# Performance work log

Hardware: AMD Instinct MI355X
Metric: run time of the kernel (lower is better)

Reference implementation:

```python
import jax, jax.numpy as jnp
import numpy as np

B, T, Nt = 64, 256, 77      # batch, motion length, text tokens
H, L = 8, 64                # num_heads, latent_dim per head
D = H * L                   # 512 model dim
Pt = 256                    # text_latent_dim
Ht = 1                      # num_text_heads
E, K = 8, 2                 # num_experts, topk
TEMB = 2048                 # time_embed_dim
MAXS, MAXTS = 512, 77       # max_seq_len, max_text_seq_len
NEG = -1e6


def _ln(x, g, b, eps=1e-5):
    m = jnp.mean(x, -1, keepdims=True)
    v = jnp.mean((x - m) ** 2, -1, keepdims=True)
    return (x - m) * jax.lax.rsqrt(v + eps) * g + b


def _gelu(x):
    return jax.nn.gelu(x, approximate=False)


def _moe_tokens(x, gate_w, fc1w, fc1b, fc2w, fc2b):
    # top-k softmax gate (fp32) + expert FFNs; dense compute, sparse combine.
    logits = x.astype(jnp.float32) @ gate_w.astype(jnp.float32)          # [Ntok,E]
    gates = jax.nn.softmax(logits, axis=-1)
    topv, topi = jax.lax.top_k(gates, K)
    topv = topv / jnp.sum(topv, -1, keepdims=True)
    dense = jnp.sum(jax.nn.one_hot(topi, E, dtype=topv.dtype) * topv[..., None], axis=1)
    dense = dense.astype(x.dtype)                                        # [Ntok,E]
    y = jnp.zeros((x.shape[0], fc2w.shape[-1]), x.dtype)
    for e in range(E):  # small fixed expert loop
        h = _gelu(x @ fc1w[e] + fc1b[e])
        y = y + dense[:, e:e + 1] * (h @ fc2w[e] + fc2b[e])
    return y


def _moe_block(x, pos, gate_w, fc1w, fc1b, fc2w, fc2b, projw, projb):
    # x: [B,Tn,Hn,Din]; add learned positional embedding, MoE over tokens, GELU, proj.
    b, t, h, d = x.shape
    x = x + pos[:, :t]
    y = _moe_tokens(x.reshape(-1, d), gate_w, fc1w, fc1b, fc2w, fc2b)
    y = _gelu(y) @ projw + projb
    return y.reshape(b, t, h, -1)


def _fwd(x, xf, emb, src_mask, norm_g, norm_b, tnorm_g, tnorm_b, m_pos, m_gate, m_fc1w, m_fc1b, m_fc2w, m_fc2b, m_projw, m_projb, t_pos, t_gate, t_fc1w, t_fc1b, t_fc2w, t_fc2b, t_projw, t_projb, body_w, sb_embw, sb_embb, sb_ng, sb_nb, sb_outw, sb_outb, cond_type):
    Bx, Tx, Dx = x.shape
    x4 = x.reshape(Bx, Tx, H, L)
    tf = xf.reshape(Bx, Nt, Ht, Pt)
    text_feat = _moe_block(_ln(tf, tnorm_g, tnorm_b), t_pos, t_gate, t_fc1w, t_fc1b, t_fc2w, t_fc2b, t_projw, t_projb)      # [B,Nt,Ht,2L]
    motion_feat = _moe_block(_ln(x4, norm_g, norm_b), m_pos, m_gate, m_fc1w, m_fc1b, m_fc2w, m_fc2b, m_projw, m_projb)      # [B,T,H,4L]
    # static body-part mixing
    bw = jax.nn.softmax(body_w, axis=1)
    body_feat = jnp.einsum('hl,bnld->bnhd', bw, motion_feat[..., :L]).reshape(Bx, Tx, Dx)
    tc = (cond_type % 10 > 0).astype(x.dtype).reshape(Bx, 1, 1, 1)
    sm = src_mask.reshape(Bx, Tx, 1, 1)
    key_text = jnp.broadcast_to(text_feat[..., :L] + (1.0 - tc) * NEG, (Bx, Nt, H, L))
    key_motion = motion_feat[..., L:2 * L] + (1.0 - sm) * NEG
    key = jax.nn.softmax(jnp.concatenate([key_text, key_motion], axis=1), axis=1)  # softmax over N
    val_text = jnp.broadcast_to(text_feat[..., L:] * tc, (Bx, Nt, H, L))
    val_motion = motion_feat[..., 2 * L:3 * L] * sm
    value = jnp.concatenate([val_text, val_motion], axis=1)                        # [B,N,H,L]
    query = jax.nn.softmax(motion_feat[..., 3 * L:], axis=-1)                      # [B,T,H,L]
    attn = jnp.einsum('bnhd,bnhl->bhdl', key, value)                               # [B,H,L,L]
    y_t = jnp.einsum('bnhd,bhdl->bnhl', query, attn).reshape(Bx, Tx, Dx)
    # StylizationBlock (eval: dropout is identity)
    h = _ln(body_feat + y_t, sb_ng, sb_nb)
    eo = jax.nn.silu(emb) @ sb_embw + sb_embb                                      # [B,2D]
    h = h * (1.0 + eo[:, None, :Dx]) + eo[:, None, Dx:]
    h = jax.nn.silu(h) @ sb_outw + sb_outb
    return x + h


def setup_inputs() -> dict:
    ks = iter(jax.random.split(jax.random.key(0), 48))
    nrm = lambda shape, s: jax.random.normal(next(ks), shape, jnp.float32) * s
    return {
        "x": nrm((B, T, D), 1.0),
        "xf": nrm((B, Nt, Pt), 1.0),
        "emb": nrm((B, TEMB), 1.0),
        "src_mask": jnp.ones((B, T, 1), jnp.float32),
        "norm_g": jnp.ones((L,), jnp.float32), "norm_b": jnp.zeros((L,), jnp.float32),
        "tnorm_g": jnp.ones((Pt,), jnp.float32), "tnorm_b": jnp.zeros((Pt,), jnp.float32),
        "m_pos": nrm((1, MAXS, H, L), 0.02),
        "m_gate": nrm((L, E), 0.02),
        "m_fc1w": nrm((E, L, 4 * L), 0.02), "m_fc1b": jnp.zeros((E, 4 * L), jnp.float32),
        "m_fc2w": nrm((E, 4 * L, L), 0.02), "m_fc2b": jnp.zeros((E, L), jnp.float32),
        "m_projw": nrm((L, 4 * L), 0.02), "m_projb": jnp.zeros((4 * L,), jnp.float32),
        "t_pos": nrm((1, MAXTS, Ht, Pt), 0.02),
        "t_gate": nrm((Pt, E), 0.02),
        "t_fc1w": nrm((E, Pt, 4 * Pt), 0.02), "t_fc1b": jnp.zeros((E, 4 * Pt), jnp.float32),
        "t_fc2w": nrm((E, 4 * Pt, Pt), 0.02), "t_fc2b": jnp.zeros((E, Pt), jnp.float32),
        "t_projw": nrm((Pt, 2 * L), 0.02), "t_projb": jnp.zeros((2 * L,), jnp.float32),
        "body_w": nrm((H, H), 1.0),
        "sb_embw": nrm((TEMB, 2 * D), 0.02), "sb_embb": jnp.zeros((2 * D,), jnp.float32),
        "sb_ng": jnp.ones((D,), jnp.float32), "sb_nb": jnp.zeros((D,), jnp.float32),
        "sb_outw": nrm((D, D), 0.02), "sb_outb": jnp.zeros((D,), jnp.float32),
        "cond_type": jax.random.randint(next(ks), (B, 1, 1), 0, 100, jnp.int32),
        "motion_length": T,
        "num_intervals": 1,
    }


def reference(x, xf, emb, src_mask, norm_g, norm_b, tnorm_g, tnorm_b, m_pos, m_gate, m_fc1w, m_fc1b, m_fc2w, m_fc2b, m_projw, m_projb, t_pos, t_gate, t_fc1w, t_fc1b, t_fc2w, t_fc2b, t_projw, t_projb, body_w, sb_embw, sb_embb, sb_ng, sb_nb, sb_outw, sb_outb, cond_type, motion_length, num_intervals):
    # motion_length / num_intervals are unused by the forward math (as in the source).
    return _fwd(x, xf, emb, src_mask, norm_g, norm_b, tnorm_g, tnorm_b, m_pos, m_gate, m_fc1w, m_fc1b, m_fc2w, m_fc2b, m_projw, m_projb, t_pos, t_gate, t_fc1w, t_fc1b, t_fc2w, t_fc2b, t_projw, t_projb, body_w, sb_embw, sb_embb, sb_ng, sb_nb, sb_outw, sb_outb, cond_type)
```

## Files before the change

kernel.cpp:

```cpp
#include <hip/hip_runtime.h>
#include <hip/hip_bf16.h>


typedef __hip_bfloat16 bf16;
typedef unsigned short u16;
typedef unsigned int   u32;
typedef __attribute__((ext_vector_type(8))) short short8;
typedef __attribute__((ext_vector_type(4))) short s16x4;
typedef __attribute__((ext_vector_type(4))) float f32x4;

#define MFMA16(a,b,c) __builtin_amdgcn_mfma_f32_16x16x32_bf16(a,b,c,0,0,0)

__device__ __forceinline__ float b2f(bf16 v){ return __bfloat162float(v); }
__device__ __forceinline__ u16 f2bu(float f){
  union { __hip_bfloat16 hh; u16 us; } cv; cv.hh = __float2bfloat16(f); return cv.us;
}
__device__ __forceinline__ float bu2f(u16 v){ return __uint_as_float(((u32)v)<<16); }

__device__ __forceinline__ float geluf(float x){
  float t = x*x;
  float w = x * fmaf(-0.10294453f, t, -2.3022077f);
  float z = exp2f(w);
  return x * __builtin_amdgcn_rcpf(1.f + z);
}
__device__ __forceinline__ float siluf(float x){
  float z = exp2f(-1.442695f * x);
  return x * __builtin_amdgcn_rcpf(1.f + z);
}

__device__ __forceinline__ float wsum(float v){
#pragma unroll
  for (int o=32;o>0;o>>=1) v += __shfl_xor(v,o,64);
  return v;
}
__device__ __forceinline__ float wmax(float v){
#pragma unroll
  for (int o=32;o>0;o>>=1) v = fmaxf(v, __shfl_xor(v,o,64));
  return v;
}
__device__ __forceinline__ void top2(const float* lg, int& i1, int& i2, float& wA){
  i1 = 0; float v1 = lg[0];
#pragma unroll
  for (int e=1;e<8;e++) if (lg[e] > v1){ v1 = lg[e]; i1 = e; }
  i2 = 0; float v2 = -1e30f;
#pragma unroll
  for (int e=0;e<8;e++) if (e != i1 && lg[e] > v2){ v2 = lg[e]; i2 = e; }
  wA = 1.f/(1.f + expf(v2 - v1));
}

__device__ __forceinline__ float sum2_wave(float x, int b0){
  float s = x, ss = x*x;
  float v = (b0 ? ss : s) + __shfl_xor(b0 ? s : ss, 1, 64);
  v += __shfl_xor(v, 2, 64);
  v += __shfl_xor(v, 4, 64);
  v += __shfl_xor(v, 8, 64);
  v += __shfl_xor(v, 16, 64);
  v += __shfl_xor(v, 32, 64);
  return v;
}

__device__ __forceinline__ float rsum8(const float p[8], int lane){
  int b0 = lane & 1, b1 = lane & 2, b2 = lane & 4;
  float w[4], u[2], v;
#pragma unroll
  for (int j=0;j<4;j++){
    float keep = b0 ? p[2*j+1] : p[2*j];
    float send = b0 ? p[2*j]   : p[2*j+1];
    w[j] = keep + __shfl_xor(send, 1, 64);
  }
#pragma unroll
  for (int i=0;i<2;i++){
    float keep = b1 ? w[2*i+1] : w[2*i];
    float send = b1 ? w[2*i]   : w[2*i+1];
    u[i] = keep + __shfl_xor(send, 2, 64);
  }
  {
    float keep = b2 ? u[1] : u[0];
    float send = b2 ? u[0] : u[1];
    v = keep + __shfl_xor(send, 4, 64);
  }
  v += __shfl_xor(v, 8, 64);
  v += __shfl_xor(v, 16, 64);
  v += __shfl_xor(v, 32, 64);
  return v;
}

__device__ __forceinline__ short8 ld8(const u16* p){
  s16x4 lo = *(const s16x4*)p;
  s16x4 hi = *(const s16x4*)(p + 4);
  short8 r;
  r[0]=lo[0]; r[1]=lo[1]; r[2]=lo[2]; r[3]=lo[3];
  r[4]=hi[0]; r[5]=hi[1]; r[6]=hi[2]; r[7]=hi[3];
  return r;
}

__global__ __launch_bounds__(64) void k_zero(int* cnts){ cnts[threadIdx.x] = 0; }

__global__ __launch_bounds__(64) void k_bw(const float* __restrict__ body_w, float* __restrict__ bwv){
  int t = threadIdx.x;
  if (t < 8){
    float v[8]; float mx = -1e30f;
#pragma unroll
    for (int j=0;j<8;j++){ v[j] = body_w[t*8+j]; mx = fmaxf(mx, v[j]); }
    float s = 0.f;
#pragma unroll
    for (int j=0;j<8;j++){ v[j] = expf(v[j]-mx); s += v[j]; }
#pragma unroll
    for (int j=0;j<8;j++) bwv[t*8+j] = v[j]/s;
  }
}

__global__ __launch_bounds__(256) void k_repack(const float* __restrict__ s, u16* __restrict__ d,
                                                int KC, int N, int total){
  int NT = N >> 4;
  for (int t = blockIdx.x*256 + threadIdx.x; t < total; t += gridDim.x*256){
    int j = t & 7, n = (t>>3) & 15, q = (t>>7) & 3;
    int r2 = t >> 9;
    int kc = r2 % KC; int r3 = r2 / KC;
    int nt = r3 % NT; int e = r3 / NT;
    int k = kc*32 + q*8 + j;
    d[t] = f2bu(s[((size_t)(e*(KC*32) + k))*N + nt*16 + n]);
  }
}

__global__ __launch_bounds__(256) void k_count(const int2* __restrict__ eidx, int n, int* __restrict__ cnt){
  __shared__ int h[8];
  int tid = threadIdx.x;
  if (tid < 8) h[tid] = 0;
  __syncthreads();
  for (int i = blockIdx.x*256 + tid; i < n; i += gridDim.x*256){
    int2 e = eidx[i];
    atomicAdd(&h[e.x], 1); atomicAdd(&h[e.y], 1);
  }
  __syncthreads();
  if (tid < 8) atomicAdd(&cnt[tid], h[tid]);
}

__global__ __launch_bounds__(64) void k_scan(int* cnts){
  if (threadIdx.x == 0){
    int s = 0;
    for (int e=0;e<8;e++){ cnts[16+e] = s; cnts[32+e] = s; s += cnts[e]; }
    s = 0;
    for (int e=0;e<8;e++){ cnts[24+e] = s; cnts[40+e] = s; s += cnts[8+e]; }
  }
}

__global__ __launch_bounds__(256) void k_fill(const int2* __restrict__ eidx, int n,
                                              int* __restrict__ off2, int* __restrict__ alist){
  __shared__ int lc[8], gb[8], lc2[8];
  int tid = threadIdx.x;
  if (tid < 8){ lc[tid] = 0; lc2[tid] = 0; }
  __syncthreads();
  for (int i = blockIdx.x*256 + tid; i < n; i += gridDim.x*256){
    int2 e = eidx[i];
    atomicAdd(&lc[e.x], 1); atomicAdd(&lc[e.y], 1);
  }
  __syncthreads();
  if (tid < 8) gb[tid] = atomicAdd(&off2[tid], lc[tid]);
  __syncthreads();
  for (int i = blockIdx.x*256 + tid; i < n; i += gridDim.x*256){
    int2 e = eidx[i];
    int s0 = atomicAdd(&lc2[e.x], 1); alist[gb[e.x] + s0] = i*2;
    int s1 = atomicAdd(&lc2[e.y], 1); alist[gb[e.y] + s1] = i*2 + 1;
  }
}

__global__ __launch_bounds__(256) void k_text_pre(
    const float* __restrict__ xf, const float* __restrict__ tg, const float* __restrict__ tb,
    const float* __restrict__ tpos, const float* __restrict__ gw,
    u16* __restrict__ xtb, int2* __restrict__ eidxT, float2* __restrict__ ewT){
  int tok = blockIdx.x, tid = threadIdx.x;
  int n = tok % 77;
  __shared__ float redw[32], lgs[8];
  int w = tid >> 6, ln = tid & 63;
  int b0 = tid & 1;
  float xv = xf[tok*256 + tid];
  float v = sum2_wave(xv, b0);
  if (ln < 2) redw[w*2 + ln] = v;
  __syncthreads();
  float mean = (redw[0]+redw[2]+redw[4]+redw[6]) * (1.f/256.f);
  float var  = (redw[1]+redw[3]+redw[5]+redw[7]) * (1.f/256.f) - mean*mean;
  float r = rsqrtf(var + 1e-5f);
  float xn = (xv - mean)*r*tg[tid] + tb[tid] + tpos[n*256 + tid];
  xtb[tok*256 + tid] = f2bu(xn);
  float p[8];
#pragma unroll
  for (int e=0;e<8;e++) p[e] = xn * gw[tid*8 + e];
  float vv = rsum8(p, ln);
  __syncthreads();
  if (ln < 8) redw[w*8 + ln] = vv;
  __syncthreads();
  if (tid < 8) lgs[tid] = redw[tid] + redw[8+tid] + redw[16+tid] + redw[24+tid];
  __syncthreads();
  if (tid == 0){
    int i1, i2; float wA; top2(lgs, i1, i2, wA);
    eidxT[tok] = make_int2(i1, i2);
    ewT[tok] = make_float2(wA, 1.f - wA);
  }
}

__global__ __launch_bounds__(256) void k_motion_pre(
    const float* __restrict__ x, const float* __restrict__ ng, const float* __restrict__ nb,
    const float* __restrict__ mpos, const float* __restrict__ gw,
    u16* __restrict__ xmb, int2* __restrict__ eidxM, float2* __restrict__ ewM){
  int tok = blockIdx.x*4 + (threadIdx.x >> 6);
  int d = threadIdx.x & 63;
  int b0 = d & 1;
  float xv = x[(size_t)tok*64 + d];
  float v = sum2_wave(xv, b0);
  float o = __shfl_xor(v, 1, 64);
  float sf  = b0 ? o : v;
  float ssf = b0 ? v : o;
  float mean = sf * (1.f/64.f);
  float var  = ssf * (1.f/64.f) - mean*mean;
  float r = rsqrtf(var + 1e-5f);
  int h = tok & 7; int t = (tok >> 3) & 255;
  float xn = (xv - mean)*r*ng[d] + nb[d] + mpos[(t*8+h)*64 + d];
  xmb[(size_t)tok*64 + d] = f2bu(xn);
  float p[8];
#pragma unroll
  for (int e=0;e<8;e++) p[e] = xn * gw[d*8 + e];
  float vv = rsum8(p, d);
  float lg[8];
#pragma unroll
  for (int e=0;e<8;e++) lg[e] = __shfl(vv, e, 64);
  if (d == 0){
    int i1, i2; float wA; top2(lg, i1, i2, wA);
    eidxM[tok] = make_int2(i1, i2);
    ewM[tok] = make_float2(wA, 1.f - wA);
  }
}

__global__ __launch_bounds__(256) void k_motion_moe(
    const u16* __restrict__ xmb, const int* __restrict__ alistM, const int* __restrict__ cnts,
    const u16* __restrict__ w1pk, const float* __restrict__ fc1b,
    const u16* __restrict__ w2pk, const float* __restrict__ fc2b,
    u16* __restrict__ ycM){
  int e = blockIdx.y, tile = blockIdx.x, tid = threadIdx.x;
  int cnt = cnts[8+e]; int base = tile*32;
  if (base >= cnt) return;
  int nn = min(32, cnt - base); int off = cnts[24+e];
  __shared__ int toks[32];
  __shared__ u16 xs[32*72];
  __shared__ u16 hT[32*264];
  if (tid < 32) toks[tid] = alistM[off + base + min(tid, nn-1)];
  __syncthreads();
  { int row = tid >> 3, c0 = (tid & 7)*8;
    short8 v = *(const short8*)(xmb + (size_t)(toks[row]>>1)*64 + c0);
    *(short8*)&xs[row*72 + c0] = v; }
  __syncthreads();
  int lane = tid & 63, w = tid >> 6;
  int n = lane & 15, q = lane >> 4;
  int mt = w & 1;
  short8 a0 = *(const short8*)&xs[(mt*16 + n)*72 + q*8];
  short8 a1 = *(const short8*)&xs[(mt*16 + n)*72 + 32 + q*8];
  const short8* b1 = (const short8*)(w1pk + (size_t)e*16384);
#pragma unroll
  for (int i=0;i<8;i++){
    int nt = (w>>1)*8 + i;
    f32x4 acc = {0.f,0.f,0.f,0.f};
    acc = MFMA16(a0, b1[(nt*2+0)*64 + lane], acc);
    acc = MFMA16(a1, b1[(nt*2+1)*64 + lane], acc);
    float bias = fc1b[e*256 + nt*16 + n];
#pragma unroll
    for (int r=0;r<4;r++)
      hT[(mt*16 + q*4 + r)*264 + nt*16 + n] = f2bu(geluf(acc[r] + bias));
  }
  __syncthreads();
  short8 a2[8];
#pragma unroll
  for (int kc=0;kc<8;kc++) a2[kc] = *(const short8*)&hT[(mt*16 + n)*264 + kc*32 + q*8];
  const short8* b2 = (const short8*)(w2pk + (size_t)e*16384);
#pragma unroll
  for (int i=0;i<2;i++){
    int nt = (w>>1)*2 + i;
    f32x4 acc = {0.f,0.f,0.f,0.f};
#pragma unroll
    for (int kc=0;kc<8;kc++) acc = MFMA16(a2[kc], b2[(nt*8+kc)*64 + lane], acc);
    float bias = fc2b[e*64 + nt*16 + n];
#pragma unroll
    for (int r=0;r<4;r++){
      int row = mt*16 + q*4 + r;
      if (row < nn) ycM[(size_t)toks[row]*64 + nt*16 + n] = f2bu(acc[r] + bias);
    }
  }
}

__global__ __launch_bounds__(256) void k_text_moe(
    const u16* __restrict__ xtb, const int* __restrict__ alistT, const int* __restrict__ cnts,
    const u16* __restrict__ w1pk, const float* __restrict__ fc1b,
    const u16* __restrict__ w2pk, const float* __restrict__ fc2b,
    float* __restrict__ ycT){
  int e = blockIdx.y, tile = blockIdx.x, tid = threadIdx.x;
  int cnt = cnts[e]; int base = tile*16;
  if (base >= cnt) return;
  int nn = min(16, cnt - base); int off = cnts[16+e];
  __shared__ int toks[16];
  __shared__ u16 xs[16*280];
  __shared__ u16 hT[16*1048];
  if (tid < 16) toks[tid] = alistT[off + base + min(tid, nn-1)];
  __syncthreads();
  { int row = tid >> 4, c0 = (tid & 15)*16;
    const short8* sp = (const short8*)(xtb + (size_t)(toks[row]>>1)*256 + c0);
    short8 v0 = sp[0], v1 = sp[1];
    *(short8*)&xs[row*280 + c0] = v0;
    *(short8*)&xs[row*280 + c0 + 8] = v1; }
  __syncthreads();
  int lane = tid & 63, w = tid >> 6;
  int n = lane & 15, q = lane >> 4;
  short8 a_[8];
#pragma unroll
  for (int kc=0;kc<8;kc++) a_[kc] = *(const short8*)&xs[n*280 + kc*32 + q*8];
  const short8* b1 = (const short8*)(w1pk + (size_t)e*262144);
#pragma unroll 1
  for (int i=0;i<16;i++){
    int nt = w*16 + i;
    f32x4 acc = {0.f,0.f,0.f,0.f};
#pragma unroll
    for (int kc=0;kc<8;kc++) acc = MFMA16(a_[kc], b1[(nt*8+kc)*64 + lane], acc);
    float bias = fc1b[e*1024 + nt*16 + n];
#pragma unroll
    for (int r=0;r<4;r++)
      hT[(q*4 + r)*1048 + nt*16 + n] = f2bu(geluf(acc[r] + bias));
  }
  __syncthreads();
  const short8* b2 = (const short8*)(w2pk + (size_t)e*262144);
  f32x4 acc[4];
#pragma unroll
  for (int i=0;i<4;i++) acc[i] = (f32x4){0.f,0.f,0.f,0.f};
#pragma unroll 1
  for (int kc=0;kc<32;kc++){
    short8 a = *(const short8*)&hT[n*1048 + kc*32 + q*8];
#pragma unroll
    for (int i=0;i<4;i++){
      int nt = w*4 + i;
      acc[i] = MFMA16(a, b2[(nt*32+kc)*64 + lane], acc[i]);
    }
  }
#pragma unroll
  for (int i=0;i<4;i++){
    int nt = w*4 + i;
    float bias = fc2b[e*256 + nt*16 + n];
#pragma unroll
    for (int r=0;r<4;r++){
      int row = q*4 + r;
      if (row < nn) ycT[(size_t)toks[row]*256 + nt*16 + n] = acc[i][r] + bias;
    }
  }
}

__global__ __launch_bounds__(128) void k_text_combine(
    const float* __restrict__ ycT, const float2* __restrict__ ewT,
    const float* __restrict__ pw, const float* __restrict__ pb,
    float* __restrict__ tfeat){
  int t = blockIdx.x, tid = threadIdx.x;
  __shared__ float gy[256];
  float2 w = ewT[t];
  for (int c=tid; c<256; c+=128){
    float y = w.x*ycT[(size_t)(t*2)*256 + c] + w.y*ycT[(size_t)(t*2+1)*256 + c];
    gy[c] = geluf(y);
  }
  __syncthreads();
  float a = pb[tid];
  for (int k=0;k<256;k++) a += gy[k] * pw[k*128 + tid];
  tfeat[(size_t)t*128 + tid] = a;
}

__global__ __launch_bounds__(256) void k_mproj(
    const u16* __restrict__ ycM, const float2* __restrict__ ewM,
    const u16* __restrict__ wpk, const float* __restrict__ pb,
    u16* __restrict__ mf, u16* __restrict__ qs){
  int t0 = blockIdx.x*32, tid = threadIdx.x;
  __shared__ u16 xs[32*72];
  { int row = tid >> 3, c0 = (tid & 7)*8;
    int tok = t0 + row;
    float2 wgt = ewM[tok];
    short8 v0 = *(const short8*)(ycM + (size_t)(tok*2)*64 + c0);
    short8 v1 = *(const short8*)(ycM + (size_t)(tok*2+1)*64 + c0);
    short8 o;
#pragma unroll
    for (int j=0;j<8;j++)
      o[j] = (short)f2bu(geluf(wgt.x*bu2f((u16)v0[j]) + wgt.y*bu2f((u16)v1[j])));
    *(short8*)&xs[row*72 + c0] = o; }
  __syncthreads();
  int lane = tid & 63, w = tid >> 6;
  int n = lane & 15, q = lane >> 4;
  int mt = w & 1;
  short8 a0 = *(const short8*)&xs[(mt*16 + n)*72 + q*8];
  short8 a1 = *(const short8*)&xs[(mt*16 + n)*72 + 32 + q*8];
  const short8* bp = (const short8*)wpk;
  float vals[4][4];
#pragma unroll
  for (int i=0;i<8;i++){
    int nt = (w>>1)*8 + i;
    f32x4 acc = {0.f,0.f,0.f,0.f};
    acc = MFMA16(a0, bp[(nt*2+0)*64 + lane], acc);
    acc = MFMA16(a1, bp[(nt*2+1)*64 + lane], acc);
    float bias = pb[nt*16 + n];
#pragma unroll
    for (int r=0;r<4;r++){
      float v = acc[r] + bias;
      if (w >= 2 && i >= 4) vals[i-4][r] = v;
      int tok = t0 + mt*16 + q*4 + r;
      mf[(size_t)tok*256 + nt*16 + n] = f2bu(v);
    }
  }
  if (w >= 2){
#pragma unroll
    for (int r=0;r<4;r++){
      int tok = t0 + mt*16 + q*4 + r;
      float m = fmaxf(fmaxf(vals[0][r], vals[1][r]), fmaxf(vals[2][r], vals[3][r]));
#pragma unroll
      for (int o=8;o>0;o>>=1) m = fmaxf(m, __shfl_xor(m, o, 64));
      float e0 = expf(vals[0][r]-m), e1 = expf(vals[1][r]-m);
      float e2 = expf(vals[2][r]-m), e3 = expf(vals[3][r]-m);
      float s = (e0+e1) + (e2+e3);
#pragma unroll
      for (int o=8;o>0;o>>=1) s += __shfl_xor(s, o, 64);
      float inv = __builtin_amdgcn_rcpf(s);
      u16* qp = qs + (size_t)tok*64 + n;
      qp[0]  = f2bu(e0*inv);
      qp[16] = f2bu(e1*inv);
      qp[32] = f2bu(e2*inv);
      qp[48] = f2bu(e3*inv);
    }
  }
}

__global__ __launch_bounds__(256) void k_eo1(const float* __restrict__ emb, const float* __restrict__ ew,
                      float* __restrict__ ep){
  int ct = blockIdx.x & 15;
  int ks = blockIdx.x >> 4;
  int tid = threadIdx.x;
  int k0 = ks*128, c0 = ct*64;
  __shared__ float aS[128*68];
  __shared__ float bS[128*64];
#pragma unroll
  for (int i=0;i<8;i++){
    int idx4 = tid + i*256;
    int b = idx4 >> 5, kq = idx4 & 31;
    f32x4 v = *(const f32x4*)(emb + (size_t)b*2048 + k0 + kq*4);
    aS[(kq*4+0)*68 + b] = siluf(v[0]);
    aS[(kq*4+1)*68 + b] = siluf(v[1]);
    aS[(kq*4+2)*68 + b] = siluf(v[2]);
    aS[(kq*4+3)*68 + b] = siluf(v[3]);
  }
#pragma unroll
  for (int i=0;i<8;i++){
    int idx4 = tid + i*256;
    int kk = idx4 >> 4, cq = idx4 & 15;
    *(f32x4*)&bS[kk*64 + cq*4] = *(const f32x4*)(ew + (size_t)(k0+kk)*1024 + c0 + cq*4);
  }
  __syncthreads();
  int cg = tid & 15, bg = tid >> 4;
  f32x4 acc[4] = {{0.f,0.f,0.f,0.f},{0.f,0.f,0.f,0.f},{0.f,0.f,0.f,0.f},{0.f,0.f,0.f,0.f}};
#pragma unroll 4
  for (int kk=0;kk<128;kk++){
    f32x4 a = *(const f32x4*)&aS[kk*68 + bg*4];
    f32x4 bb = *(const f32x4*)&bS[kk*64 + cg*4];
#pragma unroll
    for (int i=0;i<4;i++){
      acc[i][0] += a[i]*bb[0];
      acc[i][1] += a[i]*bb[1];
      acc[i][2] += a[i]*bb[2];
      acc[i][3] += a[i]*bb[3];
    }
  }
#pragma unroll
  for (int i=0;i<4;i++){
    int b = bg*4 + i;
    *(f32x4*)&ep[((size_t)(ks*64 + b))*1024 + c0 + cg*4] = acc[i];
  }
}

__global__ __launch_bounds__(256) void k_eo2(const float* __restrict__ ep, const float* __restrict__ ebias,
                      float* __restrict__ eo){
  int idx = blockIdx.x*256 + threadIdx.x;
  int c = idx & 1023;
  float s = ebias[c];
#pragma unroll
  for (int ks=0;ks<16;ks++) s += ep[(size_t)ks*65536 + idx];
  eo[idx] = s;
}

#define AT_STRIDE 364
__global__ __launch_bounds__(512) void k_attn(const float* __restrict__ tfeat, const u16* __restrict__ mf,
                       const float* __restrict__ src_mask, const int* __restrict__ cond,
                       u16* __restrict__ attnT){
  int b = blockIdx.x >> 3; int h = blockIdx.x & 7;
  int tid = threadIdx.x; int c = tid & 63; int part = tid >> 6;
  __shared__ u16 ebT[64*AT_STRIDE];
  __shared__ u16 vbT[64*AT_STRIDE];
  __shared__ float colmax[64], colsum[64], red[512];
  float tc = ((cond[b] % 10) > 0) ? 1.f : 0.f;
  float negt = (1.f - tc) * (-1e6f);

  float mx = -1e30f;
  for (int k = 0; k < 11; k++){
    int n0 = part*44 + k*4;
    s16x4 kb4, vb4;
#pragma unroll
    for (int jj = 0; jj < 4; jj++){
      int n = n0 + jj;
      float kv, vv;
      if (n < 77){
        const float* trow = tfeat + (b*77+n)*128;
        kv = trow[c] + negt;
        vv = trow[64 + c] * tc;
      } else if (n < 333){
        int t = n - 77; float smv = src_mask[b*256 + t];
        const u16* mrow = mf + ((size_t)(b*256+t)*8+h)*256;
        kv = bu2f(mrow[64 + c]) + (1.f - smv)*(-1e6f);
        vv = bu2f(mrow[128 + c]) * smv;
      } else { kv = -1e30f; vv = 0.f; }
      kb4[jj] = (short)f2bu(kv);
      vb4[jj] = (short)f2bu(vv);
      mx = fmaxf(mx, kv);
    }
    *(s16x4*)&ebT[c*AT_STRIDE + n0] = kb4;
    *(s16x4*)&vbT[c*AT_STRIDE + n0] = vb4;
  }
  red[tid] = mx; __syncthreads();
  if (part == 0){
    float m = red[c];
#pragma unroll
    for (int p=1;p<8;p++) m = fmaxf(m, red[p*64 + c]);
    colmax[c] = m;
  }
  __syncthreads();
  { int rowc = tid >> 3, j = tid & 7;
    float cm = colmax[rowc];
    float s = 0.f;
    for (int k = 0; k < 11; k++){
      int n0 = (j*11 + k)*4;
      s16x4 v4 = *(const s16x4*)&ebT[rowc*AT_STRIDE + n0];
      float e0 = expf(bu2f((u16)v4[0]) - cm);
      float e1 = expf(bu2f((u16)v4[1]) - cm);
      float e2 = expf(bu2f((u16)v4[2]) - cm);
      float e3 = expf(bu2f((u16)v4[3]) - cm);
      s += (e0+e1) + (e2+e3);
      s16x4 o;
      o[0]=(short)f2bu(e0); o[1]=(short)f2bu(e1); o[2]=(short)f2bu(e2); o[3]=(short)f2bu(e3);
      *(s16x4*)&ebT[rowc*AT_STRIDE + n0] = o;
    }
    red[tid] = s;
  }
  __syncthreads();
  if (tid < 64){
    float t2 = 0.f;
#pragma unroll
    for (int p=0;p<8;p++) t2 += red[tid*8 + p];
    colsum[tid] = t2;
  }
  __syncthreads();
  int lane = tid & 63, w = tid >> 6;
  int n16 = lane & 15, q = lane >> 4;
  int mt = w >> 1;
  int ntb = (w & 1) * 2;
  f32x4 acc0 = {0.f,0.f,0.f,0.f}, acc1 = {0.f,0.f,0.f,0.f};
  const u16* ea = &ebT[(mt*16 + n16)*AT_STRIDE + q*8];
  const u16* v0p = &vbT[(ntb*16 + n16)*AT_STRIDE + q*8];
  const u16* v1p = &vbT[((ntb+1)*16 + n16)*AT_STRIDE + q*8];
#pragma unroll
  for (int kc = 0; kc < 11; kc++){
    short8 a  = ld8(ea  + kc*32);
    short8 b0 = ld8(v0p + kc*32);
    short8 b1 = ld8(v1p + kc*32);
    acc0 = MFMA16(a, b0, acc0);
    acc1 = MFMA16(a, b1, acc1);
  }
  float inv[4];
#pragma unroll
  for (int r=0;r<4;r++) inv[r] = __builtin_amdgcn_rcpf(colsum[mt*16 + q*4 + r]);
  u16* outp = attnT + (size_t)(b*8+h)*4096;
  int d0 = mt*16 + q*4;
  {
    int l = ntb*16 + n16;
    s16x4 o;
#pragma unroll
    for (int r=0;r<4;r++) o[r] = (short)f2bu(acc0[r]*inv[r]);
    *(s16x4*)(outp + l*64 + d0) = o;
  }
  {
    int l = (ntb+1)*16 + n16;
    s16x4 o;
#pragma unroll
    for (int r=0;r<4;r++) o[r] = (short)f2bu(acc1[r]*inv[r]);
    *(s16x4*)(outp + l*64 + d0) = o;
  }
}

__global__ __launch_bounds__(256) void k_yt(const u16* __restrict__ qs, const u16* __restrict__ attnT,
                                            u16* __restrict__ yt){
  int b = blockIdx.x >> 3; int h = blockIdx.x & 7;
  int tid = threadIdx.x;
  int lane = tid & 63, w = tid >> 6;
  int n = lane & 15, q = lane >> 4;
  const u16* qsb = qs + ((size_t)(b*256)*8 + h)*64;
  const u16* ab  = attnT + (size_t)(b*8+h)*4096;
  f32x4 acc[4][4];
#pragma unroll
  for (int mt=0;mt<4;mt++)
#pragma unroll
    for (int nt=0;nt<4;nt++) acc[mt][nt] = (f32x4){0.f,0.f,0.f,0.f};
#pragma unroll
  for (int kc=0;kc<2;kc++){
    short8 a_[4], b_[4];
#pragma unroll
    for (int mt=0;mt<4;mt++){
      int t = w*64 + mt*16 + n;
      a_[mt] = *(const short8*)(qsb + (size_t)t*512 + kc*32 + q*8);
    }
#pragma unroll
    for (int nt=0;nt<4;nt++){
      int l = nt*16 + n;
      b_[nt] = *(const short8*)(ab + l*64 + kc*32 + q*8);
    }
#pragma unroll
    for (int mt=0;mt<4;mt++)
#pragma unroll
      for (int nt=0;nt<4;nt++)
        acc[mt][nt] = MFMA16(a_[mt], b_[nt], acc[mt][nt]);
  }
#pragma unroll
  for (int mt=0;mt<4;mt++)
#pragma unroll
    for (int nt=0;nt<4;nt++){
      int l = nt*16 + n;
#pragma unroll
      for (int r=0;r<4;r++){
        int t = w*64 + mt*16 + q*4 + r;
        yt[((size_t)(b*256+t)*8 + h)*64 + l] = f2bu(acc[mt][nt][r]);
      }
    }
}

__global__ __launch_bounds__(256) void k_j2(const u16* __restrict__ mf, const u16* __restrict__ yt,
                     const float* __restrict__ bwv, const float* __restrict__ eo,
                     const float* __restrict__ sb_ng, const float* __restrict__ sb_nb,
                     float* __restrict__ sbuf){
  int blk = blockIdx.x; int b = blk >> 8; int t = blk & 255;
  int tid = threadIdx.x;
  __shared__ float mfl[512], red[4];
#pragma unroll
  for (int ii=0; ii<2; ii++){
    int idx = tid + ii*256; int h = idx >> 6; int dd = idx & 63;
    mfl[idx] = bu2f(mf[((size_t)(b*256+t)*8+h)*256 + dd]);
  }
  __syncthreads();
  int w = tid >> 6, ln = tid & 63;
  float out[2];
#pragma unroll
  for (int ii=0; ii<2; ii++){
    int idx = tid + ii*256; int h = idx >> 6; int l = idx & 63;
    float a = bu2f(yt[((size_t)(b*256+t)*8 + h)*64 + l]);
    float bs = 0.f;
#pragma unroll
    for (int lh=0; lh<8; lh++) bs += bwv[h*8 + lh] * mfl[lh*64 + l];
    out[ii] = a + bs;
  }
  float psum = wsum(out[0] + out[1]);
  if (ln == 0) red[w] = psum;
  __syncthreads();
  float mean = (red[0]+red[1]+red[2]+red[3]) * (1.f/512.f);
  __syncthreads();
  float c0 = out[0]-mean, c1 = out[1]-mean;
  float pv = wsum(c0*c0 + c1*c1);
  if (ln == 0) red[w] = pv;
  __syncthreads();
  float var = (red[0]+red[1]+red[2]+red[3]) * (1.f/512.f);
  float r = rsqrtf(var + 1e-5f);
#pragma unroll
  for (int ii=0; ii<2; ii++){
    int c = tid + ii*256;
    float hn = (out[ii]-mean)*r*sb_ng[c] + sb_nb[c];
    float e1 = eo[b*1024 + c], e2 = eo[b*1024 + 512 + c];
    float hm = hn*(1.f + e1) + e2;
    sbuf[(size_t)blk*512 + c] = siluf(hm);
  }
}

__global__ __launch_bounds__(256) void k_out(const u16* __restrict__ wpk,
                      const float* __restrict__ bias, const float* __restrict__ x,
                      float* __restrict__ out){
  int r0 = blockIdx.x*32, tid = threadIdx.x;
  __shared__ u16 xs[32*536];
  { int row = tid >> 3, c0 = (tid & 7)*64;
    const f32x4* sp = (const f32x4*)(out + (size_t)(r0+row)*512 + c0);
#pragma unroll
    for (int j=0;j<8;j++){
      f32x4 va = sp[2*j], vb = sp[2*j+1];
      short8 o;
      o[0]=(short)f2bu(va[0]); o[1]=(short)f2bu(va[1]); o[2]=(short)f2bu(va[2]); o[3]=(short)f2bu(va[3]);
      o[4]=(short)f2bu(vb[0]); o[5]=(short)f2bu(vb[1]); o[6]=(short)f2bu(vb[2]); o[7]=(short)f2bu(vb[3]);
      *(short8*)&xs[row*536 + c0 + 8*j] = o;
    } }
  __syncthreads();
  int lane = tid & 63, w = tid >> 6;
  int n = lane & 15, q = lane >> 4;
  int mt = w & 1;
  short8 a_[16];
#pragma unroll
  for (int kc=0;kc<16;kc++) a_[kc] = *(const short8*)&xs[(mt*16 + n)*536 + kc*32 + q*8];
  const short8* bp = (const short8*)wpk;
#pragma unroll 1
  for (int i=0;i<16;i++){
    int nt = (w>>1)*16 + i;
    f32x4 acc = {0.f,0.f,0.f,0.f};
#pragma unroll
    for (int kc=0;kc<16;kc++) acc = MFMA16(a_[kc], bp[(nt*16+kc)*64 + lane], acc);
    int col = nt*16 + n;
    float bv = bias[col];
#pragma unroll
    for (int r=0;r<4;r++){
      size_t rowg = (size_t)(r0 + mt*16 + q*4 + r);
      out[rowg*512 + col] = acc[r] + bv + x[rowg*512 + col];
    }
  }
}

extern "C" void kernel_launch(void* const* d_in, const int* in_sizes, int n_in,
                              void* d_out, int out_size, void* d_ws, size_t ws_size,
                              hipStream_t stream) {
  (void)in_sizes; (void)n_in; (void)out_size; (void)ws_size;
  const float* x        = (const float*)d_in[0];
  const float* xf       = (const float*)d_in[1];
  const float* emb      = (const float*)d_in[2];
  const float* src_mask = (const float*)d_in[3];
  const float* norm_g   = (const float*)d_in[4];
  const float* norm_b   = (const float*)d_in[5];
  const float* tnorm_g  = (const float*)d_in[6];
  const float* tnorm_b  = (const float*)d_in[7];
  const float* m_pos    = (const float*)d_in[8];
  const float* m_gate   = (const float*)d_in[9];
  const float* m_fc1w   = (const float*)d_in[10];
  const float* m_fc1b   = (const float*)d_in[11];
  const float* m_fc2w   = (const float*)d_in[12];
  const float* m_fc2b   = (const float*)d_in[13];
  const float* m_projw  = (const float*)d_in[14];
  const float* m_projb  = (const float*)d_in[15];
  const float* t_pos    = (const float*)d_in[16];
  const float* t_gate   = (const float*)d_in[17];
  const float* t_fc1w   = (const float*)d_in[18];
  const float* t_fc1b   = (const float*)d_in[19];
  const float* t_fc2w   = (const float*)d_in[20];
  const float* t_fc2b   = (const float*)d_in[21];
  const float* t_projw  = (const float*)d_in[22];
  const float* t_projb  = (const float*)d_in[23];
  const float* body_w   = (const float*)d_in[24];
  const float* sb_embw  = (const float*)d_in[25];
  const float* sb_embb  = (const float*)d_in[26];
  const float* sb_ng    = (const float*)d_in[27];
  const float* sb_nb    = (const float*)d_in[28];
  const float* sb_outw  = (const float*)d_in[29];
  const float* sb_outb  = (const float*)d_in[30];
  const int*   cond     = (const int*)d_in[31];

  char* base = (char*)d_ws;
  size_t o = 0;
  auto alloc = [&](size_t bytes)->char*{ char* r = base + o; o += (bytes + 255) & ~(size_t)255; return r; };
  u16*  mf      = (u16*)alloc(67108864);
  char* R       = alloc(33554432);
  float* ep     = (float*)(R);
  u16*  xtb     = (u16*)(R);
  float* ycT    = (float*)(R + 4194304);
  u16*  ycM     = (u16*)(R);
  u16*  attnT   = (u16*)(R);
  u16*  yt      = (u16*)(R + 8388608);
  u16*  xmb     = (u16*)alloc(16777216);
  u16*  qs      = xmb;
  u16*  t1pk    = (u16*)alloc(4194304);
  u16*  t2pk    = (u16*)alloc(4194304);
  u16*  m1pk    = (u16*)alloc(262144);
  u16*  m2pk    = (u16*)alloc(262144);
  u16*  mppk    = (u16*)alloc(32768);
  u16*  wopk    = (u16*)alloc(524288);
  int2* eidxT   = (int2*)alloc(39424);
  float2* ewT   = (float2*)alloc(39424);
  int2* eidxM   = (int2*)alloc(1048576);
  float2* ewM   = (float2*)alloc(1048576);
  int*  alistT  = (int*)alloc(39424);
  int*  alistM  = (int*)alloc(1048576);
  int*  cnts    = (int*)alloc(256);
  float* tfeat  = (float*)alloc(2523136);
  float* eo     = (float*)alloc(262144);
  float* bwv    = (float*)alloc(256);
  float* sbuf   = (float*)d_out;

  k_zero<<<1, 64, 0, stream>>>(cnts);
  k_bw<<<1, 64, 0, stream>>>(body_w, bwv);
  k_repack<<<512, 256, 0, stream>>>(t_fc1w, t1pk, 8, 1024, 2097152);
  k_repack<<<512, 256, 0, stream>>>(t_fc2w, t2pk, 32, 256, 2097152);
  k_repack<<<64, 256, 0, stream>>>(m_fc1w, m1pk, 2, 256, 131072);
  k_repack<<<64, 256, 0, stream>>>(m_fc2w, m2pk, 8, 64, 131072);
  k_repack<<<8, 256, 0, stream>>>(m_projw, mppk, 2, 256, 16384);
  k_repack<<<128, 256, 0, stream>>>(sb_outw, wopk, 16, 512, 262144);
  k_eo1<<<256, 256, 0, stream>>>(emb, sb_embw, ep);
  k_eo2<<<256, 256, 0, stream>>>(ep, sb_embb, eo);

  k_text_pre<<<4928, 256, 0, stream>>>(xf, tnorm_g, tnorm_b, t_pos, t_gate, xtb, eidxT, ewT);
  k_motion_pre<<<32768, 256, 0, stream>>>(x, norm_g, norm_b, m_pos, m_gate, xmb, eidxM, ewM);
  k_count<<<32, 256, 0, stream>>>(eidxT, 4928, cnts);
  k_count<<<256, 256, 0, stream>>>(eidxM, 131072, cnts + 8);
  k_scan<<<1, 64, 0, stream>>>(cnts);
  k_fill<<<32, 256, 0, stream>>>(eidxT, 4928, cnts + 32, alistT);
  k_fill<<<256, 256, 0, stream>>>(eidxM, 131072, cnts + 40, alistM);

  k_text_moe<<<dim3(308, 8), 256, 0, stream>>>(xtb, alistT, cnts, t1pk, t_fc1b, t2pk, t_fc2b, ycT);
  k_text_combine<<<4928, 128, 0, stream>>>(ycT, ewT, t_projw, t_projb, tfeat);

  k_motion_moe<<<dim3(4096, 8), 256, 0, stream>>>(xmb, alistM, cnts, m1pk, m_fc1b, m2pk, m_fc2b, ycM);
  k_mproj<<<4096, 256, 0, stream>>>(ycM, ewM, mppk, m_projb, mf, qs);

  k_attn<<<512, 512, 0, stream>>>(tfeat, mf, src_mask, cond, attnT);
  k_yt<<<512, 256, 0, stream>>>(qs, attnT, yt);
  k_j2<<<16384, 256, 0, stream>>>(mf, yt, bwv, eo, sb_ng, sb_nb, sbuf);
  k_out<<<512, 256, 0, stream>>>(wopk, sb_outb, x, (float*)d_out);
}
```

Before: 520.5 us.

## Merge setup kernels, drop count/scan via per-expert fixed-stride lists, tune motion MoE

Merges the zero and softmax setup kernels into one, and folds the six weight repack launches into one flat kernel. Removes the count and scan passes by giving each expert a fixed-capacity slot region in the assignment lists, so a single fill pass both counts and places tokens. The motion MoE kernel preloads its fc1 weight fragments, swaps the MFMA operand order so each lane writes contiguous 4-element vectors for hT and the output, and adds an occupancy hint to launch_bounds. The cost is larger assignment buffers and more registers held by the preloaded weights.

```diff
diff --git a/kernel.cpp b/kernel.cpp
--- a/kernel.cpp
+++ b/kernel.cpp
@@ -94,10 +94,10 @@
   return r;
 }
 
-__global__ __launch_bounds__(64) void k_zero(int* cnts){ cnts[threadIdx.x] = 0; }
-
-__global__ __launch_bounds__(64) void k_bw(const float* __restrict__ body_w, float* __restrict__ bwv){
+__global__ __launch_bounds__(64) void k_init(int* cnts, const float* __restrict__ body_w,
+                                             float* __restrict__ bwv){
   int t = threadIdx.x;
+  cnts[t] = 0;
   if (t < 8){
     float v[8]; float mx = -1e30f;
 #pragma unroll
@@ -110,43 +110,33 @@
   }
 }
 
-__global__ __launch_bounds__(256) void k_repack(const float* __restrict__ s, u16* __restrict__ d,
-                                                int KC, int N, int total){
+__global__ __launch_bounds__(256) void k_repack_all(
+    const float* __restrict__ s0, u16* __restrict__ d0,
+    const float* __restrict__ s1, u16* __restrict__ d1,
+    const float* __restrict__ s2, u16* __restrict__ d2,
+    const float* __restrict__ s3, u16* __restrict__ d3,
+    const float* __restrict__ s4, u16* __restrict__ d4,
+    const float* __restrict__ s5, u16* __restrict__ d5){
+  long g = (long)blockIdx.x*256 + threadIdx.x;
+  if (g >= 4734976) return;
+  const float* s; u16* d; int KC, N; long t;
+  if      (g < 2097152){ s=s0; d=d0; KC=8;  N=1024; t=g; }
+  else if (g < 4194304){ s=s1; d=d1; KC=32; N=256;  t=g-2097152; }
+  else if (g < 4325376){ s=s2; d=d2; KC=2;  N=256;  t=g-4194304; }
+  else if (g < 4456448){ s=s3; d=d3; KC=8;  N=64;   t=g-4325376; }
+  else if (g < 4472832){ s=s4; d=d4; KC=2;  N=256;  t=g-4456448; }
+  else                 { s=s5; d=d5; KC=16; N=512;  t=g-4472832; }
   int NT = N >> 4;
-  for (int t = blockIdx.x*256 + threadIdx.x; t < total; t += gridDim.x*256){
-    int j = t & 7, n = (t>>3) & 15, q = (t>>7) & 3;
-    int r2 = t >> 9;
-    int kc = r2 % KC; int r3 = r2 / KC;
-    int nt = r3 % NT; int e = r3 / NT;
-    int k = kc*32 + q*8 + j;
-    d[t] = f2bu(s[((size_t)(e*(KC*32) + k))*N + nt*16 + n]);
-  }
-}
-
-__global__ __launch_bounds__(256) void k_count(const int2* __restrict__ eidx, int n, int* __restrict__ cnt){
-  __shared__ int h[8];
-  int tid = threadIdx.x;
-  if (tid < 8) h[tid] = 0;
-  __syncthreads();
-  for (int i = blockIdx.x*256 + tid; i < n; i += gridDim.x*256){
-    int2 e = eidx[i];
-    atomicAdd(&h[e.x], 1); atomicAdd(&h[e.y], 1);
-  }
-  __syncthreads();
-  if (tid < 8) atomicAdd(&cnt[tid], h[tid]);
-}
-
-__global__ __launch_bounds__(64) void k_scan(int* cnts){
-  if (threadIdx.x == 0){
-    int s = 0;
-    for (int e=0;e<8;e++){ cnts[16+e] = s; cnts[32+e] = s; s += cnts[e]; }
-    s = 0;
-    for (int e=0;e<8;e++){ cnts[24+e] = s; cnts[40+e] = s; s += cnts[8+e]; }
-  }
-}
-
-__global__ __launch_bounds__(256) void k_fill(const int2* __restrict__ eidx, int n,
-                                              int* __restrict__ off2, int* __restrict__ alist){
+  int j = t & 7, n = (t>>3) & 15, q = (t>>7) & 3;
+  long r2 = t >> 9;
+  int kc = (int)(r2 % KC); long r3 = r2 / KC;
+  int nt = (int)(r3 % NT); int e = (int)(r3 / NT);
+  int k = kc*32 + q*8 + j;
+  d[t] = f2bu(s[((size_t)(e*(KC*32) + k))*N + nt*16 + n]);
+}
+
+__global__ __launch_bounds__(256) void k_filld(const int2* __restrict__ eidx, int n, int stride,
+                                               int* __restrict__ cnt, int* __restrict__ alist){
   __shared__ int lc[8], gb[8], lc2[8];
   int tid = threadIdx.x;
   if (tid < 8){ lc[tid] = 0; lc2[tid] = 0; }
@@ -156,12 +146,12 @@
     atomicAdd(&lc[e.x], 1); atomicAdd(&lc[e.y], 1);
   }
   __syncthreads();
-  if (tid < 8) gb[tid] = atomicAdd(&off2[tid], lc[tid]);
+  if (tid < 8) gb[tid] = atomicAdd(&cnt[tid], lc[tid]);
   __syncthreads();
   for (int i = blockIdx.x*256 + tid; i < n; i += gridDim.x*256){
     int2 e = eidx[i];
-    int s0 = atomicAdd(&lc2[e.x], 1); alist[gb[e.x] + s0] = i*2;
-    int s1 = atomicAdd(&lc2[e.y], 1); alist[gb[e.y] + s1] = i*2 + 1;
+    int s0 = atomicAdd(&lc2[e.x], 1); alist[e.x*stride + gb[e.x] + s0] = i*2;
+    int s1 = atomicAdd(&lc2[e.y], 1); alist[e.y*stride + gb[e.y] + s1] = i*2 + 1;
   }
 }
 
@@ -231,7 +221,7 @@
   }
 }
 
-__global__ __launch_bounds__(256) void k_motion_moe(
+__global__ __launch_bounds__(256, 4) void k_motion_moe(
     const u16* __restrict__ xmb, const int* __restrict__ alistM, const int* __restrict__ cnts,
     const u16* __restrict__ w1pk, const float* __restrict__ fc1b,
     const u16* __restrict__ w2pk, const float* __restrict__ fc2b,
@@ -239,7 +229,7 @@
   int e = blockIdx.y, tile = blockIdx.x, tid = threadIdx.x;
   int cnt = cnts[8+e]; int base = tile*32;
   if (base >= cnt) return;
-  int nn = min(32, cnt - base); int off = cnts[24+e];
+  int nn = min(32, cnt - base); int off = e*131072;
   __shared__ int toks[32];
   __shared__ u16 xs[32*72];
   __shared__ u16 hT[32*264];
@@ -252,36 +242,47 @@
   int lane = tid & 63, w = tid >> 6;
   int n = lane & 15, q = lane >> 4;
   int mt = w & 1;
-  short8 a0 = *(const short8*)&xs[(mt*16 + n)*72 + q*8];
-  short8 a1 = *(const short8*)&xs[(mt*16 + n)*72 + 32 + q*8];
+  short8 x0 = *(const short8*)&xs[(mt*16 + n)*72 + q*8];
+  short8 x1 = *(const short8*)&xs[(mt*16 + n)*72 + 32 + q*8];
   const short8* b1 = (const short8*)(w1pk + (size_t)e*16384);
+  short8 b1f[16];
+#pragma unroll
+  for (int i=0;i<8;i++){
+    int nt = (w>>1)*8 + i;
+    b1f[2*i]   = b1[(nt*2+0)*64 + lane];
+    b1f[2*i+1] = b1[(nt*2+1)*64 + lane];
+  }
 #pragma unroll
   for (int i=0;i<8;i++){
     int nt = (w>>1)*8 + i;
     f32x4 acc = {0.f,0.f,0.f,0.f};
-    acc = MFMA16(a0, b1[(nt*2+0)*64 + lane], acc);
-    acc = MFMA16(a1, b1[(nt*2+1)*64 + lane], acc);
-    float bias = fc1b[e*256 + nt*16 + n];
-#pragma unroll
-    for (int r=0;r<4;r++)
-      hT[(mt*16 + q*4 + r)*264 + nt*16 + n] = f2bu(geluf(acc[r] + bias));
+    acc = MFMA16(b1f[2*i],   x0, acc);
+    acc = MFMA16(b1f[2*i+1], x1, acc);
+    f32x4 bias = *(const f32x4*)(fc1b + e*256 + nt*16 + q*4);
+    s16x4 o;
+#pragma unroll
+    for (int r=0;r<4;r++) o[r] = (short)f2bu(geluf(acc[r] + bias[r]));
+    *(s16x4*)&hT[(mt*16 + n)*264 + nt*16 + q*4] = o;
   }
   __syncthreads();
   short8 a2[8];
 #pragma unroll
   for (int kc=0;kc<8;kc++) a2[kc] = *(const short8*)&hT[(mt*16 + n)*264 + kc*32 + q*8];
   const short8* b2 = (const short8*)(w2pk + (size_t)e*16384);
+  bool valid = (mt*16 + n) < nn;
+  int slot = toks[mt*16 + n];
 #pragma unroll
   for (int i=0;i<2;i++){
     int nt = (w>>1)*2 + i;
     f32x4 acc = {0.f,0.f,0.f,0.f};
 #pragma unroll
-    for (int kc=0;kc<8;kc++) acc = MFMA16(a2[kc], b2[(nt*8+kc)*64 + lane], acc);
-    float bias = fc2b[e*64 + nt*16 + n];
-#pragma unroll
-    for (int r=0;r<4;r++){
-      int row = mt*16 + q*4 + r;
-      if (row < nn) ycM[(size_t)toks[row]*64 + nt*16 + n] = f2bu(acc[r] + bias);
+    for (int kc=0;kc<8;kc++) acc = MFMA16(b2[(nt*8+kc)*64 + lane], a2[kc], acc);
+    f32x4 bias = *(const f32x4*)(fc2b + e*64 + nt*16 + q*4);
+    if (valid){
+      s16x4 o;
+#pragma unroll
+      for (int r=0;r<4;r++) o[r] = (short)f2bu(acc[r] + bias[r]);
+      *(s16x4*)(ycM + (size_t)slot*64 + nt*16 + q*4) = o;
     }
   }
 }
@@ -294,7 +295,7 @@
   int e = blockIdx.y, tile = blockIdx.x, tid = threadIdx.x;
   int cnt = cnts[e]; int base = tile*16;
   if (base >= cnt) return;
-  int nn = min(16, cnt - base); int off = cnts[16+e];
+  int nn = min(16, cnt - base); int off = e*4928;
   __shared__ int toks[16];
   __shared__ u16 xs[16*280];
   __shared__ u16 hT[16*1048];
@@ -779,32 +780,24 @@
   float2* ewT   = (float2*)alloc(39424);
   int2* eidxM   = (int2*)alloc(1048576);
   float2* ewM   = (float2*)alloc(1048576);
-  int*  alistT  = (int*)alloc(39424);
-  int*  alistM  = (int*)alloc(1048576);
+  int*  alistT  = (int*)alloc(157696);
+  int*  alistM  = (int*)alloc(4194304);
   int*  cnts    = (int*)alloc(256);
   float* tfeat  = (float*)alloc(2523136);
   float* eo     = (float*)alloc(262144);
   float* bwv    = (float*)alloc(256);
   float* sbuf   = (float*)d_out;
 
-  k_zero<<<1, 64, 0, stream>>>(cnts);
-  k_bw<<<1, 64, 0, stream>>>(body_w, bwv);
-  k_repack<<<512, 256, 0, stream>>>(t_fc1w, t1pk, 8, 1024, 2097152);
-  k_repack<<<512, 256, 0, stream>>>(t_fc2w, t2pk, 32, 256, 2097152);
-  k_repack<<<64, 256, 0, stream>>>(m_fc1w, m1pk, 2, 256, 131072);
-  k_repack<<<64, 256, 0, stream>>>(m_fc2w, m2pk, 8, 64, 131072);
-  k_repack<<<8, 256, 0, stream>>>(m_projw, mppk, 2, 256, 16384);
-  k_repack<<<128, 256, 0, stream>>>(sb_outw, wopk, 16, 512, 262144);
+  k_init<<<1, 64, 0, stream>>>(cnts, body_w, bwv);
+  k_repack_all<<<18496, 256, 0, stream>>>(t_fc1w, t1pk, t_fc2w, t2pk, m_fc1w, m1pk,
+                                          m_fc2w, m2pk, m_projw, mppk, sb_outw, wopk);
   k_eo1<<<256, 256, 0, stream>>>(emb, sb_embw, ep);
   k_eo2<<<256, 256, 0, stream>>>(ep, sb_embb, eo);
 
   k_text_pre<<<4928, 256, 0, stream>>>(xf, tnorm_g, tnorm_b, t_pos, t_gate, xtb, eidxT, ewT);
   k_motion_pre<<<32768, 256, 0, stream>>>(x, norm_g, norm_b, m_pos, m_gate, xmb, eidxM, ewM);
-  k_count<<<32, 256, 0, stream>>>(eidxT, 4928, cnts);
-  k_count<<<256, 256, 0, stream>>>(eidxM, 131072, cnts + 8);
-  k_scan<<<1, 64, 0, stream>>>(cnts);
-  k_fill<<<32, 256, 0, stream>>>(eidxT, 4928, cnts + 32, alistT);
-  k_fill<<<256, 256, 0, stream>>>(eidxM, 131072, cnts + 40, alistM);
+  k_filld<<<32, 256, 0, stream>>>(eidxT, 4928, 4928, cnts, alistT);
+  k_filld<<<256, 256, 0, stream>>>(eidxM, 131072, 131072, cnts + 8, alistM);
 
   k_text_moe<<<dim3(308, 8), 256, 0, stream>>>(xtb, alistT, cnts, t1pk, t_fc1b, t2pk, t_fc2b, ycT);
   k_text_combine<<<4928, 128, 0, stream>>>(ycT, ewT, t_projw, t_projb, tfeat);
```

Measured after the change: 477.2 us (median of 2 runs). 1.09x faster.
